# Kernel optimization log

Hardware: AMD Instinct MI355X
Metric: run time of the kernel (lower is better)

The kernel has to match this reference:

```python
import jax, jax.numpy as jnp
import numpy as np

N = 100000
E = 1600000
IN, HID, OUT = 128, 128, 64


def sage_conv(x, edge_index, W_l, W_r, b):
    # PyG SAGEConv with mean aggregation:
    # out = mean_{j in N(i)} x_j @ W_l + x_i @ W_r + b
    src, dst = edge_index[0], edge_index[1]
    msgs = x[src]                                            # [E, D] gather
    summed = jax.ops.segment_sum(msgs, dst, num_segments=N)  # [N, D] scatter-add
    deg = jax.ops.segment_sum(jnp.ones((E,), x.dtype), dst, num_segments=N)
    mean = summed / jnp.maximum(deg, 1.0)[:, None]
    return mean @ W_l + x @ W_r + b


def setup_inputs() -> dict:
    key = jax.random.key(0)
    ks = jax.random.split(key, 8)
    x = jax.random.normal(ks[0], (N, IN), dtype=jnp.float32)
    edge_index = jax.random.randint(ks[1], (2, E), 0, N, dtype=jnp.int64)
    s1 = 1.0 / np.sqrt(IN)
    s2 = 1.0 / np.sqrt(HID)
    W1_l = jax.random.uniform(ks[2], (IN, HID), jnp.float32, -s1, s1)
    W1_r = jax.random.uniform(ks[3], (IN, HID), jnp.float32, -s1, s1)
    b1 = jnp.zeros((HID,), jnp.float32)
    W2_l = jax.random.uniform(ks[4], (HID, OUT), jnp.float32, -s2, s2)
    W2_r = jax.random.uniform(ks[5], (HID, OUT), jnp.float32, -s2, s2)
    b2 = jnp.zeros((OUT,), jnp.float32)
    return {"x": x, "edge_index": edge_index, "W1_l": W1_l, "W1_r": W1_r,
            "b1": b1, "W2_l": W2_l, "W2_r": W2_r, "b2": b2}


def reference(x, edge_index, W1_l, W1_r, b1, W2_l, W2_r, b2):
    h = sage_conv(x, edge_index, W1_l, W1_r, b1)
    h = jax.nn.relu(h)
    out = sage_conv(h, edge_index, W2_l, W2_r, b2)
    return out
```

## Files before the change

kernel.cpp:

```cpp
#include <hip/hip_runtime.h>

#define NN 100000
#define NE 1600000
#define KB 782
#define BSH 7
#define MAXB 4096
#define PBLK 200

#define OFF_CC    0
#define OFF_STAGE 1024
#define OFF_XB    3204096
#define OFF_XF8   9610240
#define OFF_MEANB 12813312
#define OFF_HB    19219456
#define OFF_W1LP  25625600
#define OFF_W1RP  (25625600 + 8192)
#define OFF_W2LP  (25625600 + 16384)
#define OFF_W2RP  (25625600 + 20480)

typedef __bf16 bf16x8 __attribute__((ext_vector_type(8)));
typedef float f32x4 __attribute__((ext_vector_type(4)));
typedef float f32x2 __attribute__((ext_vector_type(2)));

static __device__ __forceinline__ ushort f2bf(float f) {
    unsigned u = __float_as_uint(f);
    return (ushort)((u + 0x7fffu + ((u >> 16) & 1u)) >> 16);
}
static __device__ __forceinline__ float bflo(unsigned u) { return __uint_as_float(u << 16); }
static __device__ __forceinline__ float bfhi(unsigned u) { return __uint_as_float(u & 0xffff0000u); }

__global__ void cvt_kernel(const float* __restrict__ x, ushort* __restrict__ xb,
                           unsigned* __restrict__ xf8) {
    int i = blockIdx.x * 256 + threadIdx.x;
    float4 v = ((const float4*)x)[i];
    uint2 o;
    o.x = (unsigned)f2bf(v.x) | ((unsigned)f2bf(v.y) << 16);
    o.y = (unsigned)f2bf(v.z) | ((unsigned)f2bf(v.w) << 16);
    ((uint2*)xb)[i] = o;
    int p8 = __builtin_amdgcn_cvt_pk_fp8_f32(v.x, v.y, 0, false);
    p8 = __builtin_amdgcn_cvt_pk_fp8_f32(v.z, v.w, p8, true);
    xf8[i] = (unsigned)p8;
}

__global__ void pack_kernel(const float* __restrict__ W1l, const float* __restrict__ W1r,
                            const float* __restrict__ W2l, const float* __restrict__ W2r,
                            ushort* __restrict__ w1lp, ushort* __restrict__ w1rp,
                            ushort* __restrict__ w2lp, ushort* __restrict__ w2rp) {
    int blk = blockIdx.x;
    const float* W;
    ushort* out;
    int N, frag0;
    if (blk < 8)       { W = W1l; out = w1lp; N = 128; frag0 = blk * 4; }
    else if (blk < 16) { W = W1r; out = w1rp; N = 128; frag0 = (blk - 8) * 4; }
    else if (blk < 20) { W = W2l; out = w2lp; N = 64;  frag0 = (blk - 16) * 4; }
    else               { W = W2r; out = w2rp; N = 64;  frag0 = (blk - 20) * 4; }
    int lane = threadIdx.x & 63;
    int frag = frag0 + (threadIdx.x >> 6);
    int NT = N >> 4;
    int ktile = frag / NT, ntile = frag - ktile * NT;
    int k = ktile * 32 + (lane >> 4) * 8;
    int n = ntile * 16 + (lane & 15);
    ushort tmp[8];
#pragma unroll
    for (int j = 0; j < 8; ++j) tmp[j] = f2bf(W[(k + j) * N + n]);
    uint4 o;
    o.x = (unsigned)tmp[0] | ((unsigned)tmp[1] << 16);
    o.y = (unsigned)tmp[2] | ((unsigned)tmp[3] << 16);
    o.z = (unsigned)tmp[4] | ((unsigned)tmp[5] << 16);
    o.w = (unsigned)tmp[6] | ((unsigned)tmp[7] << 16);
    *(uint4*)&out[(frag * 64 + lane) * 8] = o;
}

__global__ __launch_bounds__(1024) void cpart_kernel(const int* __restrict__ src,
                                                     const int* __restrict__ dst,
                                                     int* __restrict__ cc,
                                                     unsigned* __restrict__ stage) {
    __shared__ int hist[KB];
    __shared__ int cur[KB];
    int t = threadIdx.x;
    int e0 = blockIdx.x * (NE / PBLK);
    int e1 = e0 + (NE / PBLK);
    for (int i = t; i < KB; i += 1024) hist[i] = 0;
    __syncthreads();
    for (int e = e0 + t; e < e1; e += 1024)
        atomicAdd(&hist[dst[e] >> BSH], 1);
    __syncthreads();
    for (int i = t; i < KB; i += 1024) {
        int c = hist[i];
        cur[i] = c ? atomicAdd(&cc[i], c) : 0;
    }
    __syncthreads();
    for (int e = e0 + t; e < e1; e += 1024) {
        int d = dst[e];
        int bkt = d >> BSH;
        int p = atomicAdd(&cur[bkt], 1);
        if (p < MAXB)
            stage[bkt * MAXB + p] = ((unsigned)(d & 127) << 17) | (unsigned)src[e];
    }
}

__global__ __launch_bounds__(256) void agg1f_kernel(const unsigned* __restrict__ stage,
                                                    const int* __restrict__ cc,
                                                    const unsigned* __restrict__ xf8,
                                                    ushort* __restrict__ meanb) {
    __shared__ unsigned ssrc[MAXB];
    __shared__ int sc[128];
    __shared__ int loff[129];
    __shared__ int lcur[128];
    int t = threadIdx.x;
    int b = blockIdx.x;
    const unsigned* st = stage + b * MAXB;
    int cnt = min(cc[b], MAXB);

    if (t < 128) lcur[t] = 0;
    __syncthreads();
    for (int i = t; i < cnt; i += 256) atomicAdd(&lcur[st[i] >> 17], 1);
    __syncthreads();
    if (t < 128) sc[t] = lcur[t];
    __syncthreads();
    for (int off = 1; off < 128; off <<= 1) {
        int v = (t < 128 && t >= off) ? sc[t - off] : 0;
        __syncthreads();
        if (t < 128) sc[t] += v;
        __syncthreads();
    }
    if (t < 128) {
        int excl = (t == 0) ? 0 : sc[t - 1];
        loff[t] = excl;
        lcur[t] = excl;
    }
    if (t == 127) loff[128] = sc[127];
    __syncthreads();
    for (int i = t; i < cnt; i += 256) {
        unsigned v = st[i];
        int p = atomicAdd(&lcur[v >> 17], 1);
        ssrc[p] = v & 0x1FFFFu;
    }
    __syncthreads();

    int qw = t >> 4, l4 = t & 15;
    int node0 = b << BSH;
    int nmax = min(128, NN - node0);
    const uint2* xv = (const uint2*)xf8;
    for (int nl = qw; nl < nmax; nl += 16) {
        int s0 = loff[nl], s1 = loff[nl + 1];
        float a0 = 0.f, a1 = 0.f, a2 = 0.f, a3 = 0.f;
        float a4 = 0.f, a5 = 0.f, a6 = 0.f, a7 = 0.f;
        int e = s0;
        for (; e + 4 <= s1; e += 4) {
            uint2 u0 = xv[ssrc[e + 0] * 16 + l4];
            uint2 u1 = xv[ssrc[e + 1] * 16 + l4];
            uint2 u2 = xv[ssrc[e + 2] * 16 + l4];
            uint2 u3 = xv[ssrc[e + 3] * 16 + l4];
#pragma unroll
            for (int j = 0; j < 4; ++j) {
                unsigned lo = (j == 0) ? u0.x : (j == 1) ? u1.x : (j == 2) ? u2.x : u3.x;
                unsigned hi = (j == 0) ? u0.y : (j == 1) ? u1.y : (j == 2) ? u2.y : u3.y;
                f32x2 p0 = __builtin_amdgcn_cvt_pk_f32_fp8(lo, false);
                f32x2 p1 = __builtin_amdgcn_cvt_pk_f32_fp8(lo, true);
                f32x2 p2 = __builtin_amdgcn_cvt_pk_f32_fp8(hi, false);
                f32x2 p3 = __builtin_amdgcn_cvt_pk_f32_fp8(hi, true);
                a0 += p0.x; a1 += p0.y; a2 += p1.x; a3 += p1.y;
                a4 += p2.x; a5 += p2.y; a6 += p3.x; a7 += p3.y;
            }
        }
        for (; e < s1; ++e) {
            uint2 u = xv[ssrc[e] * 16 + l4];
            f32x2 p0 = __builtin_amdgcn_cvt_pk_f32_fp8(u.x, false);
            f32x2 p1 = __builtin_amdgcn_cvt_pk_f32_fp8(u.x, true);
            f32x2 p2 = __builtin_amdgcn_cvt_pk_f32_fp8(u.y, false);
            f32x2 p3 = __builtin_amdgcn_cvt_pk_f32_fp8(u.y, true);
            a0 += p0.x; a1 += p0.y; a2 += p1.x; a3 += p1.y;
            a4 += p2.x; a5 += p2.y; a6 += p3.x; a7 += p3.y;
        }
        float inv = 1.0f / fmaxf((float)(s1 - s0), 1.0f);
        uint4 o;
        o.x = (unsigned)f2bf(a0 * inv) | ((unsigned)f2bf(a1 * inv) << 16);
        o.y = (unsigned)f2bf(a2 * inv) | ((unsigned)f2bf(a3 * inv) << 16);
        o.z = (unsigned)f2bf(a4 * inv) | ((unsigned)f2bf(a5 * inv) << 16);
        o.w = (unsigned)f2bf(a6 * inv) | ((unsigned)f2bf(a7 * inv) << 16);
        *(uint4*)&meanb[(node0 + nl) * 128 + 8 * l4] = o;
    }
}

__global__ __launch_bounds__(256) void agg2f_kernel(const unsigned* __restrict__ stage,
                                                    const int* __restrict__ cc,
                                                    const ushort* __restrict__ pb,
                                                    float* __restrict__ meanp) {
    __shared__ unsigned ssrc[MAXB];
    __shared__ int sc[128];
    __shared__ int loff[129];
    __shared__ int lcur[128];
    int t = threadIdx.x;
    int b = blockIdx.x;
    const unsigned* st = stage + b * MAXB;
    int cnt = min(cc[b], MAXB);

    if (t < 128) lcur[t] = 0;
    __syncthreads();
    for (int i = t; i < cnt; i += 256) atomicAdd(&lcur[st[i] >> 17], 1);
    __syncthreads();
    if (t < 128) sc[t] = lcur[t];
    __syncthreads();
    for (int off = 1; off < 128; off <<= 1) {
        int v = (t < 128 && t >= off) ? sc[t - off] : 0;
        __syncthreads();
        if (t < 128) sc[t] += v;
        __syncthreads();
    }
    if (t < 128) {
        int excl = (t == 0) ? 0 : sc[t - 1];
        loff[t] = excl;
        lcur[t] = excl;
    }
    if (t == 127) loff[128] = sc[127];
    __syncthreads();
    for (int i = t; i < cnt; i += 256) {
        unsigned v = st[i];
        int p = atomicAdd(&lcur[v >> 17], 1);
        ssrc[p] = v & 0x1FFFFu;
    }
    __syncthreads();

    int hw = t >> 5, l5 = t & 31;
    int node0 = b << BSH;
    int nmax = min(128, NN - node0);
    const unsigned* pbu = (const unsigned*)pb;
    for (int nl = hw; nl < nmax; nl += 8) {
        int s0 = loff[nl], s1 = loff[nl + 1];
        float a0 = 0.f, a1 = 0.f;
        int e = s0;
        for (; e + 4 <= s1; e += 4) {
            unsigned u0 = pbu[ssrc[e + 0] * 32 + l5];
            unsigned u1 = pbu[ssrc[e + 1] * 32 + l5];
            unsigned u2 = pbu[ssrc[e + 2] * 32 + l5];
            unsigned u3 = pbu[ssrc[e + 3] * 32 + l5];
            a0 += bflo(u0) + bflo(u1) + bflo(u2) + bflo(u3);
            a1 += bfhi(u0) + bfhi(u1) + bfhi(u2) + bfhi(u3);
        }
        for (; e < s1; ++e) {
            unsigned u = pbu[ssrc[e] * 32 + l5];
            a0 += bflo(u); a1 += bfhi(u);
        }
        float inv = 1.0f / fmaxf((float)(s1 - s0), 1.0f);
        float2 o = {a0 * inv, a1 * inv};
        *(float2*)&meanp[(node0 + nl) * 64 + 2 * l5] = o;
    }
}

__global__ __launch_bounds__(256) void gemm1_kernel(const ushort* __restrict__ meanb,
                                                    const ushort* __restrict__ xb,
                                                    const ushort* __restrict__ w1lp,
                                                    const ushort* __restrict__ w1rp,
                                                    const float* __restrict__ b1,
                                                    const ushort* __restrict__ w2lp,
                                                    ushort* __restrict__ hb,
                                                    ushort* __restrict__ pb) {
    __shared__ ushort As[64 * 136];
    int t = threadIdx.x;
    int node0 = blockIdx.x * 64;
    int w = t >> 6, l = t & 63;
    int lrow = w * 16 + (l & 15);
    int lkq = (l >> 4) * 8;
    int cq = l & 15, rq = (l >> 4) * 4;

    f32x4 acc[8];
#pragma unroll
    for (int i = 0; i < 8; ++i) acc[i] = (f32x4){0.f, 0.f, 0.f, 0.f};

    {
        const uint4* g = (const uint4*)(meanb + (size_t)node0 * 128);
#pragma unroll
        for (int i = 0; i < 4; ++i) {
            int chunk = t + 256 * i;
            *(uint4*)&As[(chunk >> 4) * 136 + (chunk & 15) * 8] = g[chunk];
        }
    }
    __syncthreads();
#pragma unroll
    for (int kt = 0; kt < 4; ++kt) {
        bf16x8 a = *(const bf16x8*)&As[lrow * 136 + kt * 32 + lkq];
        const bf16x8* bp = (const bf16x8*)w1lp + (kt * 8) * 64 + l;
#pragma unroll
        for (int nt = 0; nt < 8; ++nt)
            acc[nt] = __builtin_amdgcn_mfma_f32_16x16x32_bf16(a, bp[nt * 64], acc[nt], 0, 0, 0);
    }
    __syncthreads();

    {
        const uint4* g = (const uint4*)(xb + (size_t)node0 * 128);
#pragma unroll
        for (int i = 0; i < 4; ++i) {
            int chunk = t + 256 * i;
            *(uint4*)&As[(chunk >> 4) * 136 + (chunk & 15) * 8] = g[chunk];
        }
    }
    __syncthreads();
#pragma unroll
    for (int kt = 0; kt < 4; ++kt) {
        bf16x8 a = *(const bf16x8*)&As[lrow * 136 + kt * 32 + lkq];
        const bf16x8* bp = (const bf16x8*)w1rp + (kt * 8) * 64 + l;
#pragma unroll
        for (int nt = 0; nt < 8; ++nt)
            acc[nt] = __builtin_amdgcn_mfma_f32_16x16x32_bf16(a, bp[nt * 64], acc[nt], 0, 0, 0);
    }
    __syncthreads();

#pragma unroll
    for (int nt = 0; nt < 8; ++nt) {
        int n = nt * 16 + cq;
        float bias = b1[n];
#pragma unroll
        for (int r = 0; r < 4; ++r) {
            float hv = fmaxf(acc[nt][r] + bias, 0.0f);
            As[(w * 16 + rq + r) * 136 + n] = f2bf(hv);
        }
    }
    __syncthreads();

    {
        uint4* g = (uint4*)(hb + (size_t)node0 * 128);
#pragma unroll
        for (int i = 0; i < 4; ++i) {
            int chunk = t + 256 * i;
            if (node0 + (chunk >> 4) < NN)
                g[chunk] = *(const uint4*)&As[(chunk >> 4) * 136 + (chunk & 15) * 8];
        }
    }

    f32x4 acc2[4];
#pragma unroll
    for (int i = 0; i < 4; ++i) acc2[i] = (f32x4){0.f, 0.f, 0.f, 0.f};
#pragma unroll
    for (int kt = 0; kt < 4; ++kt) {
        bf16x8 a = *(const bf16x8*)&As[lrow * 136 + kt * 32 + lkq];
        const bf16x8* bp = (const bf16x8*)w2lp + (kt * 4) * 64 + l;
#pragma unroll
        for (int nt = 0; nt < 4; ++nt)
            acc2[nt] = __builtin_amdgcn_mfma_f32_16x16x32_bf16(a, bp[nt * 64], acc2[nt], 0, 0, 0);
    }
    __syncthreads();

#pragma unroll
    for (int nt = 0; nt < 4; ++nt)
#pragma unroll
        for (int r = 0; r < 4; ++r)
            As[(w * 16 + rq + r) * 136 + nt * 16 + cq] = f2bf(acc2[nt][r]);
    __syncthreads();
    {
        uint4* g = (uint4*)(pb + (size_t)node0 * 64);
#pragma unroll
        for (int i = 0; i < 2; ++i) {
            int chunk = t + 256 * i;
            if (node0 + (chunk >> 3) < NN)
                g[chunk] = *(const uint4*)&As[(chunk >> 3) * 136 + (chunk & 7) * 8];
        }
    }
}

__global__ __launch_bounds__(256) void gemm2_kernel(const float* __restrict__ meanp,
                                                    const ushort* __restrict__ hb,
                                                    const ushort* __restrict__ w2rp,
                                                    const float* __restrict__ b2,
                                                    float* __restrict__ out) {
    __shared__ ushort As[64 * 136];
    int t = threadIdx.x;
    int node0 = blockIdx.x * 64;
    int w = t >> 6, l = t & 63;
    int lrow = w * 16 + (l & 15);
    int lkq = (l >> 4) * 8;
    int cq = l & 15, rq = (l >> 4) * 4;

    {
        const uint4* g = (const uint4*)(hb + (size_t)node0 * 128);
#pragma unroll
        for (int i = 0; i < 4; ++i) {
            int chunk = t + 256 * i;
            *(uint4*)&As[(chunk >> 4) * 136 + (chunk & 15) * 8] = g[chunk];
        }
    }
    __syncthreads();

    f32x4 acc[4];
#pragma unroll
    for (int i = 0; i < 4; ++i) acc[i] = (f32x4){0.f, 0.f, 0.f, 0.f};
#pragma unroll
    for (int kt = 0; kt < 4; ++kt) {
        bf16x8 a = *(const bf16x8*)&As[lrow * 136 + kt * 32 + lkq];
        const bf16x8* bp = (const bf16x8*)w2rp + (kt * 4) * 64 + l;
#pragma unroll
        for (int nt = 0; nt < 4; ++nt)
            acc[nt] = __builtin_amdgcn_mfma_f32_16x16x32_bf16(a, bp[nt * 64], acc[nt], 0, 0, 0);
    }

#pragma unroll
    for (int nt = 0; nt < 4; ++nt) {
        int n = nt * 16 + cq;
        float bias = b2[n];
#pragma unroll
        for (int r = 0; r < 4; ++r) {
            int row = node0 + w * 16 + rq + r;
            if (row < NN)
                out[(size_t)row * 64 + n] = acc[nt][r] + bias + meanp[(size_t)row * 64 + n];
        }
    }
}

extern "C" void kernel_launch(void* const* d_in, const int* in_sizes, int n_in,
                              void* d_out, int out_size, void* d_ws, size_t ws_size,
                              hipStream_t stream) {
    const float* x   = (const float*)d_in[0];
    const int*   ei  = (const int*)d_in[1];
    const float* W1l = (const float*)d_in[2];
    const float* W1r = (const float*)d_in[3];
    const float* b1  = (const float*)d_in[4];
    const float* W2l = (const float*)d_in[5];
    const float* W2r = (const float*)d_in[6];
    const float* b2  = (const float*)d_in[7];

    const int* src = ei;
    const int* dst = ei + NE;

    int*      ws_i  = (int*)d_ws;
    int*      cc    = ws_i + OFF_CC;
    unsigned* stage = (unsigned*)(ws_i + OFF_STAGE);
    ushort*   xb    = (ushort*)(ws_i + OFF_XB);
    unsigned* xf8   = (unsigned*)(ws_i + OFF_XF8);
    ushort*   pb    = (ushort*)(ws_i + OFF_XF8);
    ushort*   meanb = (ushort*)(ws_i + OFF_MEANB);
    float*    meanp = (float*)(ws_i + OFF_MEANB);
    ushort*   hb    = (ushort*)(ws_i + OFF_HB);
    ushort*   w1lp  = (ushort*)(ws_i + OFF_W1LP);
    ushort*   w1rp  = (ushort*)(ws_i + OFF_W1RP);
    ushort*   w2lp  = (ushort*)(ws_i + OFF_W2LP);
    ushort*   w2rp  = (ushort*)(ws_i + OFF_W2RP);

    hipMemsetAsync(cc, 0, 1024 * sizeof(int), stream);
    cvt_kernel<<<12500, 256, 0, stream>>>(x, xb, xf8);
    pack_kernel<<<24, 256, 0, stream>>>(W1l, W1r, W2l, W2r, w1lp, w1rp, w2lp, w2rp);
    cpart_kernel<<<PBLK, 1024, 0, stream>>>(src, dst, cc, stage);

    agg1f_kernel<<<KB, 256, 0, stream>>>(stage, cc, xf8, meanb);
    gemm1_kernel<<<(NN + 63) / 64, 256, 0, stream>>>(meanb, xb, w1lp, w1rp, b1, w2lp, hb, pb);

    agg2f_kernel<<<KB, 256, 0, stream>>>(stage, cc, pb, meanp);
    gemm2_kernel<<<(NN + 63) / 64, 256, 0, stream>>>(meanp, hb, w2rp, b2, (float*)d_out);
}
```

Before: 280.5 us.

## Materialize per-node CSR once and aggregate with fine-grained node-parallel grids

Adds a sort kernel that does the per-bucket local counting sort once, writes the sorted sources back into the staging buffer, and records each node's start and degree. Both aggregation kernels then read this CSR directly and launch one small thread group per node across many more blocks (NN/16 and NN/8). This removes the sort being repeated in both layers, lifts the large shared-memory footprint that capped occupancy, and improves load balance across CUs. In exchange it adds a global write and read of the sorted edge list, extra rstart/rdeg loads, and one more kernel launch.

Measured after the change: 271.0 us. -3.4%, faster.

```diff
diff --git a/kernel.cpp b/kernel.cpp
--- a/kernel.cpp
+++ b/kernel.cpp
@@ -8,15 +8,17 @@
 #define PBLK 200
 
 #define OFF_CC    0
-#define OFF_STAGE 1024
-#define OFF_XB    3204096
-#define OFF_XF8   9610240
-#define OFF_MEANB 12813312
-#define OFF_HB    19219456
-#define OFF_W1LP  25625600
-#define OFF_W1RP  (25625600 + 8192)
-#define OFF_W2LP  (25625600 + 16384)
-#define OFF_W2RP  (25625600 + 20480)
+#define OFF_RST   1024
+#define OFF_RDG   101120
+#define OFF_STAGE 201216
+#define OFF_XB    3404288
+#define OFF_XF8   9810432
+#define OFF_MEANB 13013504
+#define OFF_HB    19419648
+#define OFF_W1LP  25825792
+#define OFF_W1RP  (25825792 + 8192)
+#define OFF_W2LP  (25825792 + 16384)
+#define OFF_W2RP  (25825792 + 20480)
 
 typedef __bf16 bf16x8 __attribute__((ext_vector_type(8)));
 typedef float f32x4 __attribute__((ext_vector_type(4)));
@@ -99,17 +101,17 @@
     }
 }
 
-__global__ __launch_bounds__(256) void agg1f_kernel(const unsigned* __restrict__ stage,
-                                                    const int* __restrict__ cc,
-                                                    const unsigned* __restrict__ xf8,
-                                                    ushort* __restrict__ meanb) {
+__global__ __launch_bounds__(256) void sort_kernel(unsigned* __restrict__ stage,
+                                                   const int* __restrict__ cc,
+                                                   int* __restrict__ rstart,
+                                                   int* __restrict__ rdeg) {
     __shared__ unsigned ssrc[MAXB];
     __shared__ int sc[128];
     __shared__ int loff[129];
     __shared__ int lcur[128];
     int t = threadIdx.x;
     int b = blockIdx.x;
-    const unsigned* st = stage + b * MAXB;
+    unsigned* st = stage + b * MAXB;
     int cnt = min(cc[b], MAXB);
 
     if (t < 128) lcur[t] = 0;
@@ -137,115 +139,95 @@
         ssrc[p] = v & 0x1FFFFu;
     }
     __syncthreads();
-
-    int qw = t >> 4, l4 = t & 15;
+    for (int i = t; i < cnt; i += 256) st[i] = ssrc[i];
     int node0 = b << BSH;
-    int nmax = min(128, NN - node0);
+    if (t < 128 && node0 + t < NN) {
+        rstart[node0 + t] = b * MAXB + loff[t];
+        rdeg[node0 + t] = loff[t + 1] - loff[t];
+    }
+}
+
+__global__ __launch_bounds__(256) void agg1g_kernel(const unsigned* __restrict__ es,
+                                                    const int* __restrict__ rstart,
+                                                    const int* __restrict__ rdeg,
+                                                    const unsigned* __restrict__ xf8,
+                                                    ushort* __restrict__ meanb) {
+    int t = threadIdx.x;
+    int node = blockIdx.x * 16 + (t >> 4);
+    int l4 = t & 15;
+    int s0 = rstart[node];
+    int deg = rdeg[node];
     const uint2* xv = (const uint2*)xf8;
-    for (int nl = qw; nl < nmax; nl += 16) {
-        int s0 = loff[nl], s1 = loff[nl + 1];
-        float a0 = 0.f, a1 = 0.f, a2 = 0.f, a3 = 0.f;
-        float a4 = 0.f, a5 = 0.f, a6 = 0.f, a7 = 0.f;
-        int e = s0;
-        for (; e + 4 <= s1; e += 4) {
-            uint2 u0 = xv[ssrc[e + 0] * 16 + l4];
-            uint2 u1 = xv[ssrc[e + 1] * 16 + l4];
-            uint2 u2 = xv[ssrc[e + 2] * 16 + l4];
-            uint2 u3 = xv[ssrc[e + 3] * 16 + l4];
-#pragma unroll
-            for (int j = 0; j < 4; ++j) {
-                unsigned lo = (j == 0) ? u0.x : (j == 1) ? u1.x : (j == 2) ? u2.x : u3.x;
-                unsigned hi = (j == 0) ? u0.y : (j == 1) ? u1.y : (j == 2) ? u2.y : u3.y;
-                f32x2 p0 = __builtin_amdgcn_cvt_pk_f32_fp8(lo, false);
-                f32x2 p1 = __builtin_amdgcn_cvt_pk_f32_fp8(lo, true);
-                f32x2 p2 = __builtin_amdgcn_cvt_pk_f32_fp8(hi, false);
-                f32x2 p3 = __builtin_amdgcn_cvt_pk_f32_fp8(hi, true);
-                a0 += p0.x; a1 += p0.y; a2 += p1.x; a3 += p1.y;
-                a4 += p2.x; a5 += p2.y; a6 += p3.x; a7 += p3.y;
-            }
-        }
-        for (; e < s1; ++e) {
-            uint2 u = xv[ssrc[e] * 16 + l4];
-            f32x2 p0 = __builtin_amdgcn_cvt_pk_f32_fp8(u.x, false);
-            f32x2 p1 = __builtin_amdgcn_cvt_pk_f32_fp8(u.x, true);
-            f32x2 p2 = __builtin_amdgcn_cvt_pk_f32_fp8(u.y, false);
-            f32x2 p3 = __builtin_amdgcn_cvt_pk_f32_fp8(u.y, true);
+    float a0 = 0.f, a1 = 0.f, a2 = 0.f, a3 = 0.f;
+    float a4 = 0.f, a5 = 0.f, a6 = 0.f, a7 = 0.f;
+    int e = 0;
+    for (; e + 4 <= deg; e += 4) {
+        int q0 = es[s0 + e + 0];
+        int q1 = es[s0 + e + 1];
+        int q2 = es[s0 + e + 2];
+        int q3 = es[s0 + e + 3];
+        uint2 u0 = xv[q0 * 16 + l4];
+        uint2 u1 = xv[q1 * 16 + l4];
+        uint2 u2 = xv[q2 * 16 + l4];
+        uint2 u3 = xv[q3 * 16 + l4];
+#pragma unroll
+        for (int j = 0; j < 4; ++j) {
+            unsigned lo = (j == 0) ? u0.x : (j == 1) ? u1.x : (j == 2) ? u2.x : u3.x;
+            unsigned hi = (j == 0) ? u0.y : (j == 1) ? u1.y : (j == 2) ? u2.y : u3.y;
+            f32x2 p0 = __builtin_amdgcn_cvt_pk_f32_fp8(lo, false);
+            f32x2 p1 = __builtin_amdgcn_cvt_pk_f32_fp8(lo, true);
+            f32x2 p2 = __builtin_amdgcn_cvt_pk_f32_fp8(hi, false);
+            f32x2 p3 = __builtin_amdgcn_cvt_pk_f32_fp8(hi, true);
             a0 += p0.x; a1 += p0.y; a2 += p1.x; a3 += p1.y;
             a4 += p2.x; a5 += p2.y; a6 += p3.x; a7 += p3.y;
         }
-        float inv = 1.0f / fmaxf((float)(s1 - s0), 1.0f);
-        uint4 o;
-        o.x = (unsigned)f2bf(a0 * inv) | ((unsigned)f2bf(a1 * inv) << 16);
-        o.y = (unsigned)f2bf(a2 * inv) | ((unsigned)f2bf(a3 * inv) << 16);
-        o.z = (unsigned)f2bf(a4 * inv) | ((unsigned)f2bf(a5 * inv) << 16);
-        o.w = (unsigned)f2bf(a6 * inv) | ((unsigned)f2bf(a7 * inv) << 16);
-        *(uint4*)&meanb[(node0 + nl) * 128 + 8 * l4] = o;
-    }
-}
-
-__global__ __launch_bounds__(256) void agg2f_kernel(const unsigned* __restrict__ stage,
-                                                    const int* __restrict__ cc,
+    }
+    for (; e < deg; ++e) {
+        uint2 u = xv[es[s0 + e] * 16 + l4];
+        f32x2 p0 = __builtin_amdgcn_cvt_pk_f32_fp8(u.x, false);
+        f32x2 p1 = __builtin_amdgcn_cvt_pk_f32_fp8(u.x, true);
+        f32x2 p2 = __builtin_amdgcn_cvt_pk_f32_fp8(u.y, false);
+        f32x2 p3 = __builtin_amdgcn_cvt_pk_f32_fp8(u.y, true);
+        a0 += p0.x; a1 += p0.y; a2 += p1.x; a3 += p1.y;
+        a4 += p2.x; a5 += p2.y; a6 += p3.x; a7 += p3.y;
+    }
+    float inv = 1.0f / fmaxf((float)deg, 1.0f);
+    uint4 o;
+    o.x = (unsigned)f2bf(a0 * inv) | ((unsigned)f2bf(a1 * inv) << 16);
+    o.y = (unsigned)f2bf(a2 * inv) | ((unsigned)f2bf(a3 * inv) << 16);
+    o.z = (unsigned)f2bf(a4 * inv) | ((unsigned)f2bf(a5 * inv) << 16);
+    o.w = (unsigned)f2bf(a6 * inv) | ((unsigned)f2bf(a7 * inv) << 16);
+    *(uint4*)&meanb[node * 128 + 8 * l4] = o;
+}
+
+__global__ __launch_bounds__(256) void agg2g_kernel(const unsigned* __restrict__ es,
+                                                    const int* __restrict__ rstart,
+                                                    const int* __restrict__ rdeg,
                                                     const ushort* __restrict__ pb,
                                                     float* __restrict__ meanp) {
-    __shared__ unsigned ssrc[MAXB];
-    __shared__ int sc[128];
-    __shared__ int loff[129];
-    __shared__ int lcur[128];
-    int t = threadIdx.x;
-    int b = blockIdx.x;
-    const unsigned* st = stage + b * MAXB;
-    int cnt = min(cc[b], MAXB);
-
-    if (t < 128) lcur[t] = 0;
-    __syncthreads();
-    for (int i = t; i < cnt; i += 256) atomicAdd(&lcur[st[i] >> 17], 1);
-    __syncthreads();
-    if (t < 128) sc[t] = lcur[t];
-    __syncthreads();
-    for (int off = 1; off < 128; off <<= 1) {
-        int v = (t < 128 && t >= off) ? sc[t - off] : 0;
-        __syncthreads();
-        if (t < 128) sc[t] += v;
-        __syncthreads();
-    }
-    if (t < 128) {
-        int excl = (t == 0) ? 0 : sc[t - 1];
-        loff[t] = excl;
-        lcur[t] = excl;
-    }
-    if (t == 127) loff[128] = sc[127];
-    __syncthreads();
-    for (int i = t; i < cnt; i += 256) {
-        unsigned v = st[i];
-        int p = atomicAdd(&lcur[v >> 17], 1);
-        ssrc[p] = v & 0x1FFFFu;
-    }
-    __syncthreads();
-
-    int hw = t >> 5, l5 = t & 31;
-    int node0 = b << BSH;
-    int nmax = min(128, NN - node0);
+    int t = threadIdx.x;
+    int node = blockIdx.x * 8 + (t >> 5);
+    int l5 = t & 31;
+    int s0 = rstart[node];
+    int deg = rdeg[node];
     const unsigned* pbu = (const unsigned*)pb;
-    for (int nl = hw; nl < nmax; nl += 8) {
-        int s0 = loff[nl], s1 = loff[nl + 1];
-        float a0 = 0.f, a1 = 0.f;
-        int e = s0;
-        for (; e + 4 <= s1; e += 4) {
-            unsigned u0 = pbu[ssrc[e + 0] * 32 + l5];
-            unsigned u1 = pbu[ssrc[e + 1] * 32 + l5];
-            unsigned u2 = pbu[ssrc[e + 2] * 32 + l5];
-            unsigned u3 = pbu[ssrc[e + 3] * 32 + l5];
-            a0 += bflo(u0) + bflo(u1) + bflo(u2) + bflo(u3);
-            a1 += bfhi(u0) + bfhi(u1) + bfhi(u2) + bfhi(u3);
-        }
-        for (; e < s1; ++e) {
-            unsigned u = pbu[ssrc[e] * 32 + l5];
-            a0 += bflo(u); a1 += bfhi(u);
-        }
-        float inv = 1.0f / fmaxf((float)(s1 - s0), 1.0f);
-        float2 o = {a0 * inv, a1 * inv};
-        *(float2*)&meanp[(node0 + nl) * 64 + 2 * l5] = o;
-    }
+    float a0 = 0.f, a1 = 0.f;
+    int e = 0;
+    for (; e + 4 <= deg; e += 4) {
+        unsigned u0 = pbu[es[s0 + e + 0] * 32 + l5];
+        unsigned u1 = pbu[es[s0 + e + 1] * 32 + l5];
+        unsigned u2 = pbu[es[s0 + e + 2] * 32 + l5];
+        unsigned u3 = pbu[es[s0 + e + 3] * 32 + l5];
+        a0 += bflo(u0) + bflo(u1) + bflo(u2) + bflo(u3);
+        a1 += bfhi(u0) + bfhi(u1) + bfhi(u2) + bfhi(u3);
+    }
+    for (; e < deg; ++e) {
+        unsigned u = pbu[es[s0 + e] * 32 + l5];
+        a0 += bflo(u); a1 += bfhi(u);
+    }
+    float inv = 1.0f / fmaxf((float)deg, 1.0f);
+    float2 o = {a0 * inv, a1 * inv};
+    *(float2*)&meanp[node * 64 + 2 * l5] = o;
 }
 
 __global__ __launch_bounds__(256) void gemm1_kernel(const ushort* __restrict__ meanb,
@@ -421,28 +403,31 @@
     const int* src = ei;
     const int* dst = ei + NE;
 
-    int*      ws_i  = (int*)d_ws;
-    int*      cc    = ws_i + OFF_CC;
-    unsigned* stage = (unsigned*)(ws_i + OFF_STAGE);
-    ushort*   xb    = (ushort*)(ws_i + OFF_XB);
-    unsigned* xf8   = (unsigned*)(ws_i + OFF_XF8);
-    ushort*   pb    = (ushort*)(ws_i + OFF_XF8);
-    ushort*   meanb = (ushort*)(ws_i + OFF_MEANB);
-    float*    meanp = (float*)(ws_i + OFF_MEANB);
-    ushort*   hb    = (ushort*)(ws_i + OFF_HB);
-    ushort*   w1lp  = (ushort*)(ws_i + OFF_W1LP);
-    ushort*   w1rp  = (ushort*)(ws_i + OFF_W1RP);
-    ushort*   w2lp  = (ushort*)(ws_i + OFF_W2LP);
-    ushort*   w2rp  = (ushort*)(ws_i + OFF_W2RP);
+    int*      ws_i   = (int*)d_ws;
+    int*      cc     = ws_i + OFF_CC;
+    int*      rstart = ws_i + OFF_RST;
+    int*      rdeg   = ws_i + OFF_RDG;
+    unsigned* stage  = (unsigned*)(ws_i + OFF_STAGE);
+    ushort*   xb     = (ushort*)(ws_i + OFF_XB);
+    unsigned* xf8    = (unsigned*)(ws_i + OFF_XF8);
+    ushort*   pb     = (ushort*)(ws_i + OFF_XF8);
+    ushort*   meanb  = (ushort*)(ws_i + OFF_MEANB);
+    float*    meanp  = (float*)(ws_i + OFF_MEANB);
+    ushort*   hb     = (ushort*)(ws_i + OFF_HB);
+    ushort*   w1lp   = (ushort*)(ws_i + OFF_W1LP);
+    ushort*   w1rp   = (ushort*)(ws_i + OFF_W1RP);
+    ushort*   w2lp   = (ushort*)(ws_i + OFF_W2LP);
+    ushort*   w2rp   = (ushort*)(ws_i + OFF_W2RP);
 
     hipMemsetAsync(cc, 0, 1024 * sizeof(int), stream);
     cvt_kernel<<<12500, 256, 0, stream>>>(x, xb, xf8);
     pack_kernel<<<24, 256, 0, stream>>>(W1l, W1r, W2l, W2r, w1lp, w1rp, w2lp, w2rp);
     cpart_kernel<<<PBLK, 1024, 0, stream>>>(src, dst, cc, stage);
-
-    agg1f_kernel<<<KB, 256, 0, stream>>>(stage, cc, xf8, meanb);
+    sort_kernel<<<KB, 256, 0, stream>>>(stage, cc, rstart, rdeg);
+
+    agg1g_kernel<<<NN / 16, 256, 0, stream>>>(stage, rstart, rdeg, xf8, meanb);
     gemm1_kernel<<<(NN + 63) / 64, 256, 0, stream>>>(meanb, xb, w1lp, w1rp, b1, w2lp, hb, pb);
 
-    agg2f_kernel<<<KB, 256, 0, stream>>>(stage, cc, pb, meanp);
+    agg2g_kernel<<<NN / 8, 256, 0, stream>>>(stage, rstart, rdeg, pb, meanp);
     gemm2_kernel<<<(NN + 63) / 64, 256, 0, stream>>>(meanp, hb, w2rp, b2, (float*)d_out);
 }
```
